# Kernel optimization log

Measured on AMD Instinct MI355X. Metric: run time of the kernel, lower is better.

Reference implementation:

```python
import jax, jax.numpy as jnp
import numpy as np

B, N, D, C, T = 1, 262144, 64, 10, 4096
ALPHA, BETA, GAMMA = 1.0, 1.0, 1.0


def setup_inputs() -> dict:
    key = jax.random.key(0)
    ks = jax.random.split(key, 8)
    gt_img = jax.random.uniform(ks[0], (B, N, 3), jnp.float32)
    inr_output = jax.random.uniform(ks[1], (B, N, 3), jnp.float32)
    seg_output = jax.random.normal(ks[2], (B, N, C), jnp.float32)
    labels = jax.random.randint(ks[3], (B, N), 0, C)
    gt_seg = jax.nn.one_hot(labels, C, dtype=jnp.float32)  # soft-target CE layout [B,N,C]
    inr_features = jax.random.normal(ks[4], (B, N, D), jnp.float32)
    anchor_idx = jax.random.randint(ks[5], (T,), 0, N)
    pos_idx = jax.random.randint(ks[6], (T,), 0, N)
    neg_idx = jax.random.randint(ks[7], (T,), 0, N)
    return {"gt_img": gt_img, "gt_seg": gt_seg, "inr_output": inr_output,
            "seg_output": seg_output, "inr_features": inr_features,
            "anchor_idx": anchor_idx, "pos_idx": pos_idx, "neg_idx": neg_idx}


def reference(gt_img, gt_seg, inr_output, seg_output, inr_features,
              anchor_idx, pos_idx, neg_idx):
    # MSE over all elements
    mse_loss = jnp.mean((inr_output - gt_img) ** 2)
    # CrossEntropy with probability targets, mean over B*N positions
    logp = jax.nn.log_softmax(seg_output, axis=-1)  # [B,N,C]
    ce_loss = -jnp.mean(jnp.sum(gt_seg * logp, axis=-1))
    # Triplet: torch.norm over the full [B,D] slice per triplet -> reduce axes (0,2)
    a = inr_features[:, anchor_idx, :]  # [B,T,D]
    p = inr_features[:, pos_idx, :]
    n = inr_features[:, neg_idx, :]
    d_pos = jnp.sqrt(jnp.sum((a - p) ** 2, axis=(0, 2)))  # [T]
    d_neg = jnp.sqrt(jnp.sum((a - n) ** 2, axis=(0, 2)))  # [T]
    triplet_loss = jnp.sum(jax.nn.relu(d_pos - d_neg))
    return ALPHA * mse_loss + BETA * ce_loss + GAMMA * triplet_loss
```

## Files before the change

kernel.cpp:

```cpp
#include <hip/hip_runtime.h>
#include <math.h>

constexpr int N_PIX   = 262144;
constexpr int C_CLS   = 10;
constexpr int D_FEAT  = 64;
constexpr int T_TRIP  = 4096;
constexpr float ALPHA = 1.0f, BETA = 1.0f, GAMMA = 1.0f;

constexpr int MSE_F4       = N_PIX * 3 / 4;
constexpr int MSE_BLOCKS   = MSE_F4 / 256;
constexpr int CE_BLOCKS    = N_PIX / 256;
constexpr int TRIP_BLOCKS  = T_TRIP / 4;
constexpr int TOTAL_BLOCKS = MSE_BLOCKS + CE_BLOCKS + TRIP_BLOCKS;

__global__ __launch_bounds__(256) void loss_kernel(
    const float* __restrict__ gt_img,
    const float* __restrict__ gt_seg,
    const float* __restrict__ inr_out,
    const float* __restrict__ seg_out,
    const float* __restrict__ feat,
    const int*   __restrict__ aidx,
    const int*   __restrict__ pidx,
    const int*   __restrict__ nidx,
    float*       __restrict__ out)
{
    __shared__ float s_seg[256 * C_CLS];
    __shared__ float s_gt [256 * C_CLS];
    __shared__ float s_red[4];

    const int b   = blockIdx.x;
    const int tid = threadIdx.x;
    float local = 0.0f;

    if (b < MSE_BLOCKS) {
        const int i = b * 256 + tid;
        const float4 a = ((const float4*)inr_out)[i];
        const float4 g = ((const float4*)gt_img)[i];
        const float dx = a.x - g.x, dy = a.y - g.y, dz = a.z - g.z, dw = a.w - g.w;
        local = (dx*dx + dy*dy + dz*dz + dw*dw) * (ALPHA / (float)(N_PIX * 3));
    } else if (b < MSE_BLOCKS + CE_BLOCKS) {
        const int row0 = (b - MSE_BLOCKS) * 256;
        const int base = row0 * C_CLS;
        #pragma unroll
        for (int k = 0; k < C_CLS; ++k) {
            s_seg[tid + k * 256] = seg_out[base + tid + k * 256];
            s_gt [tid + k * 256] = gt_seg [base + tid + k * 256];
        }
        __syncthreads();
        const float* x = &s_seg[tid * C_CLS];
        const float* g = &s_gt [tid * C_CLS];
        float m = x[0];
        #pragma unroll
        for (int c = 1; c < C_CLS; ++c) m = fmaxf(m, x[c]);
        float s = 0.f, dot = 0.f;
        #pragma unroll
        for (int c = 0; c < C_CLS; ++c) {
            s   += __expf(x[c] - m);
            dot += g[c] * x[c];
        }
        const float lse = m + __logf(s);
        local = (lse - dot) * (BETA / (float)N_PIX);
    } else {
        const int t    = (b - MSE_BLOCKS - CE_BLOCKS) * 4 + (tid >> 6);
        const int lane = tid & 63;
        const int ai = aidx[t], pi = pidx[t], ni = nidx[t];
        const float a = feat[ai * D_FEAT + lane];
        const float p = feat[pi * D_FEAT + lane];
        const float n = feat[ni * D_FEAT + lane];
        float dp = (a - p) * (a - p);
        float dn = (a - n) * (a - n);
        #pragma unroll
        for (int off = 32; off > 0; off >>= 1) {
            dp += __shfl_down(dp, off, 64);
            dn += __shfl_down(dn, off, 64);
        }
        if (lane == 0)
            local = fmaxf(sqrtf(dp) - sqrtf(dn), 0.0f) * GAMMA;
    }

    #pragma unroll
    for (int off = 32; off > 0; off >>= 1)
        local += __shfl_down(local, off, 64);
    if ((tid & 63) == 0) s_red[tid >> 6] = local;
    __syncthreads();
    if (tid == 0)
        atomicAdd(out, s_red[0] + s_red[1] + s_red[2] + s_red[3]);
}

extern "C" void kernel_launch(void* const* d_in, const int* in_sizes, int n_in,
                              void* d_out, int out_size, void* d_ws, size_t ws_size,
                              hipStream_t stream) {
    const float* gt_img      = (const float*)d_in[0];
    const float* gt_seg      = (const float*)d_in[1];
    const float* inr_output  = (const float*)d_in[2];
    const float* seg_output  = (const float*)d_in[3];
    const float* inr_feats   = (const float*)d_in[4];
    const int*   anchor_idx  = (const int*)d_in[5];
    const int*   pos_idx     = (const int*)d_in[6];
    const int*   neg_idx     = (const int*)d_in[7];
    float* out = (float*)d_out;

    hipMemsetAsync(out, 0, sizeof(float), stream);

    loss_kernel<<<TOTAL_BLOCKS, 256, 0, stream>>>(
        gt_img, gt_seg, inr_output, seg_output, inr_feats,
        anchor_idx, pos_idx, neg_idx, out);
}
```

Before: 149.7 us.

## Spread final reduction over strided atomic slots with last-block finalize, reorder work

Block partial sums now go to 32 strided workspace accumulators instead of one global float, which cuts same-address atomic contention. A completion counter lets the last block sum the slots and write the output. Other changes in the same edit: triplet blocks are scheduled first so the latency-bound gathers start early, MSE blocks each handle two float4s per thread, and CE tiles are loaded into shared memory with float4 loads. The cost is one extra atomic per block plus a fence and a second barrier, and the single-block finish depends on the workspace being zeroed before launch.

Result: slower. 189.7 us (+26.7%).

```diff
diff --git a/kernel.cpp b/kernel.cpp
--- a/kernel.cpp
+++ b/kernel.cpp
@@ -8,10 +8,12 @@
 constexpr float ALPHA = 1.0f, BETA = 1.0f, GAMMA = 1.0f;
 
 constexpr int MSE_F4       = N_PIX * 3 / 4;
-constexpr int MSE_BLOCKS   = MSE_F4 / 256;
+constexpr int MSE_BLOCKS   = MSE_F4 / 512;
 constexpr int CE_BLOCKS    = N_PIX / 256;
 constexpr int TRIP_BLOCKS  = T_TRIP / 4;
-constexpr int TOTAL_BLOCKS = MSE_BLOCKS + CE_BLOCKS + TRIP_BLOCKS;
+constexpr int TOTAL_BLOCKS = TRIP_BLOCKS + MSE_BLOCKS + CE_BLOCKS;
+
+constexpr int NACC = 32;
 
 __global__ __launch_bounds__(256) void loss_kernel(
     const float* __restrict__ gt_img,
@@ -22,29 +24,52 @@
     const int*   __restrict__ aidx,
     const int*   __restrict__ pidx,
     const int*   __restrict__ nidx,
+    float*       __restrict__ ws,
     float*       __restrict__ out)
 {
     __shared__ float s_seg[256 * C_CLS];
     __shared__ float s_gt [256 * C_CLS];
     __shared__ float s_red[4];
+    __shared__ int   s_last;
 
     const int b   = blockIdx.x;
     const int tid = threadIdx.x;
     float local = 0.0f;
 
-    if (b < MSE_BLOCKS) {
-        const int i = b * 256 + tid;
-        const float4 a = ((const float4*)inr_out)[i];
-        const float4 g = ((const float4*)gt_img)[i];
-        const float dx = a.x - g.x, dy = a.y - g.y, dz = a.z - g.z, dw = a.w - g.w;
-        local = (dx*dx + dy*dy + dz*dz + dw*dw) * (ALPHA / (float)(N_PIX * 3));
-    } else if (b < MSE_BLOCKS + CE_BLOCKS) {
-        const int row0 = (b - MSE_BLOCKS) * 256;
-        const int base = row0 * C_CLS;
+    if (b < TRIP_BLOCKS) {
+        const int t    = b * 4 + (tid >> 6);
+        const int lane = tid & 63;
+        const int ai = aidx[t], pi = pidx[t], ni = nidx[t];
+        const float a = feat[ai * D_FEAT + lane];
+        const float p = feat[pi * D_FEAT + lane];
+        const float n = feat[ni * D_FEAT + lane];
+        float dp = (a - p) * (a - p);
+        float dn = (a - n) * (a - n);
         #pragma unroll
-        for (int k = 0; k < C_CLS; ++k) {
-            s_seg[tid + k * 256] = seg_out[base + tid + k * 256];
-            s_gt [tid + k * 256] = gt_seg [base + tid + k * 256];
+        for (int off = 32; off > 0; off >>= 1) {
+            dp += __shfl_down(dp, off, 64);
+            dn += __shfl_down(dn, off, 64);
+        }
+        if (lane == 0)
+            local = fmaxf(sqrtf(dp) - sqrtf(dn), 0.0f) * GAMMA;
+    } else if (b < TRIP_BLOCKS + MSE_BLOCKS) {
+        const int i0 = (b - TRIP_BLOCKS) * 512 + tid;
+        const float4 a0 = ((const float4*)inr_out)[i0];
+        const float4 g0 = ((const float4*)gt_img)[i0];
+        const float4 a1 = ((const float4*)inr_out)[i0 + 256];
+        const float4 g1 = ((const float4*)gt_img)[i0 + 256];
+        const float dx0 = a0.x - g0.x, dy0 = a0.y - g0.y, dz0 = a0.z - g0.z, dw0 = a0.w - g0.w;
+        const float dx1 = a1.x - g1.x, dy1 = a1.y - g1.y, dz1 = a1.z - g1.z, dw1 = a1.w - g1.w;
+        local = (dx0*dx0 + dy0*dy0 + dz0*dz0 + dw0*dw0 +
+                 dx1*dx1 + dy1*dy1 + dz1*dz1 + dw1*dw1) * (ALPHA / (float)(N_PIX * 3));
+    } else {
+        const int base4 = (b - TRIP_BLOCKS - MSE_BLOCKS) * (256 * C_CLS / 4);
+        const float4* seg4 = (const float4*)seg_out;
+        const float4* gt4  = (const float4*)gt_seg;
+        #pragma unroll
+        for (int i = tid; i < 256 * C_CLS / 4; i += 256) {
+            ((float4*)s_seg)[i] = seg4[base4 + i];
+            ((float4*)s_gt )[i] = gt4 [base4 + i];
         }
         __syncthreads();
         const float* x = &s_seg[tid * C_CLS];
@@ -60,22 +85,6 @@
         }
         const float lse = m + __logf(s);
         local = (lse - dot) * (BETA / (float)N_PIX);
-    } else {
-        const int t    = (b - MSE_BLOCKS - CE_BLOCKS) * 4 + (tid >> 6);
-        const int lane = tid & 63;
-        const int ai = aidx[t], pi = pidx[t], ni = nidx[t];
-        const float a = feat[ai * D_FEAT + lane];
-        const float p = feat[pi * D_FEAT + lane];
-        const float n = feat[ni * D_FEAT + lane];
-        float dp = (a - p) * (a - p);
-        float dn = (a - n) * (a - n);
-        #pragma unroll
-        for (int off = 32; off > 0; off >>= 1) {
-            dp += __shfl_down(dp, off, 64);
-            dn += __shfl_down(dn, off, 64);
-        }
-        if (lane == 0)
-            local = fmaxf(sqrtf(dp) - sqrtf(dn), 0.0f) * GAMMA;
     }
 
     #pragma unroll
@@ -83,8 +92,23 @@
         local += __shfl_down(local, off, 64);
     if ((tid & 63) == 0) s_red[tid >> 6] = local;
     __syncthreads();
-    if (tid == 0)
-        atomicAdd(out, s_red[0] + s_red[1] + s_red[2] + s_red[3]);
+
+    if (tid == 0) {
+        const float part = s_red[0] + s_red[1] + s_red[2] + s_red[3];
+        atomicAdd(&ws[b & (NACC - 1)], part);
+        __threadfence();
+        const unsigned old = atomicAdd((unsigned*)(ws + NACC), 1u);
+        s_last = (old == (unsigned)(TOTAL_BLOCKS - 1));
+    }
+    __syncthreads();
+
+    if (s_last && tid < 64) {
+        float v = (tid < NACC) ? atomicAdd(&ws[tid], 0.0f) : 0.0f;
+        #pragma unroll
+        for (int off = 32; off > 0; off >>= 1)
+            v += __shfl_down(v, off, 64);
+        if (tid == 0) out[0] = v;
+    }
 }
 
 extern "C" void kernel_launch(void* const* d_in, const int* in_sizes, int n_in,
@@ -99,10 +123,11 @@
     const int*   pos_idx     = (const int*)d_in[6];
     const int*   neg_idx     = (const int*)d_in[7];
     float* out = (float*)d_out;
+    float* ws  = (float*)d_ws;
 
-    hipMemsetAsync(out, 0, sizeof(float), stream);
+    hipMemsetAsync(ws, 0, (NACC + 1) * sizeof(float), stream);
 
     loss_kernel<<<TOTAL_BLOCKS, 256, 0, stream>>>(
         gt_img, gt_seg, inr_output, seg_output, inr_feats,
-        anchor_idx, pos_idx, neg_idx, out);
+        anchor_idx, pos_idx, neg_idx, ws, out);
 }
```
